# Kernel optimization log

Measured on AMD Instinct MI355X. Metric: run time of the kernel, lower is better.

## Reference

```python
import jax, jax.numpy as jnp
import numpy as np

D_MODEL = 1024
HEAD_SIZE = 64
BLOCK_SIZE = 2048
B, T = 4, 2048


def setup_inputs() -> dict:
    key = jax.random.key(0)
    ks = jax.random.split(key, 7)
    s = 1.0 / np.sqrt(D_MODEL)
    x = jax.random.normal(ks[0], (B, T, D_MODEL), dtype=jnp.float32)
    Wq = jax.random.uniform(ks[1], (D_MODEL, HEAD_SIZE), jnp.float32, -s, s)
    bq = jax.random.uniform(ks[2], (HEAD_SIZE,), jnp.float32, -s, s)
    Wk = jax.random.uniform(ks[3], (D_MODEL, HEAD_SIZE), jnp.float32, -s, s)
    bk = jax.random.uniform(ks[4], (HEAD_SIZE,), jnp.float32, -s, s)
    Wv = jax.random.uniform(ks[5], (D_MODEL, HEAD_SIZE), jnp.float32, -s, s)
    return {"x": x, "Wq": Wq, "bq": bq, "Wk": Wk, "bk": bk, "Wv": Wv, "mask": 1}


def reference(x, Wq, bq, Wk, bk, Wv, mask):
    # x: [B, T, C]; single attention head, dropout is identity (eval/p=0)
    Tlen = x.shape[1]
    q = x @ Wq + bq              # [B, T, hs]
    k = x @ Wk + bk              # [B, T, hs]
    v = x @ Wv                   # [B, T, hs] (no bias)
    hs = k.shape[-1]
    # Faithful to source: weights = QK^T / hs**(-0.5)  ==  QK^T * sqrt(hs)
    w = jnp.einsum('btd,bsd->bts', q, k) * jnp.sqrt(jnp.asarray(hs, x.dtype))
    if mask:
        causal = jnp.tril(jnp.ones((Tlen, Tlen), dtype=bool))
        w = jnp.where(causal, w, jnp.asarray(-jnp.inf, w.dtype))
    w = jax.nn.softmax(w, axis=-1)
    out = jnp.einsum('bts,bsd->btd', w, v)  # [B, T, hs]
    return out
```

## Files before the change

kernel.cpp:

```cpp
#include <hip/hip_runtime.h>
#include <hip/hip_bf16.h>

#define D_MODEL 1024
#define HS 64
#define T_LEN 2048
#define JCH 256
#define NCH 8

typedef __attribute__((ext_vector_type(8))) short bf16x8;
typedef __attribute__((ext_vector_type(4))) float f32x4;

__device__ inline void split8(const float* v, int4& hi, int4& lo) {
    union { unsigned short u[8]; int4 v4; } uh, ul;
    #pragma unroll
    for (int i = 0; i < 8; ++i) {
        const unsigned int b = __float_as_uint(v[i]);
        const unsigned short h = (unsigned short)(b >> 16);
        const float r = v[i] - __uint_as_float((unsigned int)h << 16);
        uh.u[i] = h;
        ul.u[i] = (unsigned short)(__float_as_uint(r) >> 16);
    }
    hi = uh.v4; lo = ul.v4;
}

__device__ inline unsigned short f2bf_rne(float f) {
    const unsigned int b = __float_as_uint(f);
    return (unsigned short)((b + 0x7FFFu + ((b >> 16) & 1u)) >> 16);
}
__device__ inline float bf2f(unsigned short h) {
    return __uint_as_float((unsigned int)h << 16);
}

__global__ __launch_bounds__(256) void wprep_kernel(
    const float* __restrict__ Wq, const float* __restrict__ Wk,
    const float* __restrict__ Wv, short* __restrict__ Wh, short* __restrict__ Wl)
{
    __shared__ float tile[64][69];
    const int tid = threadIdx.x;
    const int kb = blockIdx.x & 15;
    const int m  = blockIdx.x >> 4;
    const float* W = (m == 0) ? Wq : (m == 1) ? Wk : Wv;
    #pragma unroll
    for (int it = 0; it < 4; ++it) {
        const int idx = tid + 256 * it;
        const int kr = idx >> 4, c4 = idx & 15;
        *(float4*)&tile[kr][4 * c4] =
            *(const float4*)(W + (size_t)(kb * 64 + kr) * HS + 4 * c4);
    }
    __syncthreads();
    #pragma unroll
    for (int it = 0; it < 2; ++it) {
        const int s = tid + 256 * it;
        const int n = s >> 3, kc = s & 7;
        float v[8];
        #pragma unroll
        for (int i = 0; i < 8; ++i) v[i] = tile[kc * 8 + i][n];
        int4 hi, lo;
        split8(v, hi, lo);
        const size_t off = (size_t)(m * 64 + n) * D_MODEL + kb * 64 + kc * 8;
        *(int4*)(Wh + off) = hi;
        *(int4*)(Wl + off) = lo;
    }
}

__global__ __launch_bounds__(256, 3) void qkv_kernel(
    const float* __restrict__ x,
    const short* __restrict__ Wh, const short* __restrict__ Wl,
    const float* __restrict__ bq, const float* __restrict__ bk,
    float* __restrict__ q, float* __restrict__ k, float* __restrict__ vt, int BT)
{
    __shared__ __align__(16) short Ah[4 * 520], Al[4 * 520];
    __shared__ __align__(16) short Bh[8 * 520], Bl[8 * 520];

    const int tid  = threadIdx.x;
    const int r0   = blockIdx.x * 32;
    const int nb   = blockIdx.y;
    const int wave = tid >> 6;
    const int lane = tid & 63;
    const int mt_w = wave >> 1;
    const int nt0  = (wave & 1) * 2;

    f32x4 acc0 = (f32x4)(0.f);
    f32x4 acc1 = (f32x4)(0.f);

    const int amt = tid >> 7, akc = (tid >> 6) & 1, aln = tid & 63;
    const float* axsrc =
        x + (size_t)(r0 + amt * 16 + (aln & 15)) * D_MODEL + akc * 32 + (aln >> 4) * 8;

    const int b0nt = tid >> 7, b0kc = (tid >> 6) & 1, b0ln = tid & 63;
    const size_t b0off =
        (size_t)(nb * 64 + b0nt * 16 + (b0ln & 15)) * D_MODEL + b0kc * 32 + (b0ln >> 4) * 8;
    const int b1nt = 2 + (tid >> 7);
    const size_t b1off =
        (size_t)(nb * 64 + b1nt * 16 + (b0ln & 15)) * D_MODEL + b0kc * 32 + (b0ln >> 4) * 8;

    float4 a0v = *(const float4*)(axsrc);
    float4 a1v = *(const float4*)(axsrc + 4);
    int4 pb0h = *(const int4*)(Wh + b0off);
    int4 pb0l = *(const int4*)(Wl + b0off);
    int4 pb1h = *(const int4*)(Wh + b1off);
    int4 pb1l = *(const int4*)(Wl + b1off);

    for (int k0 = 0; k0 < D_MODEL; k0 += 64) {
        __syncthreads();
        {
            float xv[8];
            *(float4*)&xv[0] = a0v;
            *(float4*)&xv[4] = a1v;
            int4 hi, lo;
            split8(xv, hi, lo);
            *(int4*)&Ah[(amt * 2 + akc) * 520 + aln * 8] = hi;
            *(int4*)&Al[(amt * 2 + akc) * 520 + aln * 8] = lo;
        }
        *(int4*)&Bh[(b0nt * 2 + b0kc) * 520 + b0ln * 8] = pb0h;
        *(int4*)&Bl[(b0nt * 2 + b0kc) * 520 + b0ln * 8] = pb0l;
        *(int4*)&Bh[(b1nt * 2 + b0kc) * 520 + b0ln * 8] = pb1h;
        *(int4*)&Bl[(b1nt * 2 + b0kc) * 520 + b0ln * 8] = pb1l;
        __syncthreads();
        const int kn = k0 + 64;
        if (kn < D_MODEL) {
            a0v = *(const float4*)(axsrc + kn);
            a1v = *(const float4*)(axsrc + kn + 4);
            pb0h = *(const int4*)(Wh + b0off + kn);
            pb0l = *(const int4*)(Wl + b0off + kn);
            pb1h = *(const int4*)(Wh + b1off + kn);
            pb1l = *(const int4*)(Wl + b1off + kn);
        }
        #pragma unroll
        for (int kc = 0; kc < 2; ++kc) {
            const bf16x8 afh = *(const bf16x8*)&Ah[(mt_w * 2 + kc) * 520 + lane * 8];
            const bf16x8 afl = *(const bf16x8*)&Al[(mt_w * 2 + kc) * 520 + lane * 8];
            {
                const bf16x8 bfh = *(const bf16x8*)&Bh[(nt0 * 2 + kc) * 520 + lane * 8];
                const bf16x8 bfl = *(const bf16x8*)&Bl[(nt0 * 2 + kc) * 520 + lane * 8];
                acc0 = __builtin_amdgcn_mfma_f32_16x16x32_bf16(afh, bfh, acc0, 0, 0, 0);
                acc0 = __builtin_amdgcn_mfma_f32_16x16x32_bf16(afh, bfl, acc0, 0, 0, 0);
                acc0 = __builtin_amdgcn_mfma_f32_16x16x32_bf16(afl, bfh, acc0, 0, 0, 0);
            }
            {
                const bf16x8 bfh = *(const bf16x8*)&Bh[((nt0 + 1) * 2 + kc) * 520 + lane * 8];
                const bf16x8 bfl = *(const bf16x8*)&Bl[((nt0 + 1) * 2 + kc) * 520 + lane * 8];
                acc1 = __builtin_amdgcn_mfma_f32_16x16x32_bf16(afh, bfh, acc1, 0, 0, 0);
                acc1 = __builtin_amdgcn_mfma_f32_16x16x32_bf16(afh, bfl, acc1, 0, 0, 0);
                acc1 = __builtin_amdgcn_mfma_f32_16x16x32_bf16(afl, bfh, acc1, 0, 0, 0);
            }
        }
    }

    const int rowb = r0 + mt_w * 16 + (lane >> 4) * 4;
    #pragma unroll
    for (int j = 0; j < 2; ++j) {
        const f32x4 a = (j == 0) ? acc0 : acc1;
        const int c = nb * 64 + (nt0 + j) * 16 + (lane & 15);
        if (c < 64) {
            const float bias = bq[c];
            #pragma unroll
            for (int r = 0; r < 4; ++r)
                q[(size_t)(rowb + r) * HS + c] = a[r] + bias;
        } else if (c < 128) {
            const float bias = bk[c - 64];
            #pragma unroll
            for (int r = 0; r < 4; ++r)
                k[(size_t)(rowb + r) * HS + (c - 64)] = a[r] + bias;
        } else {
            float4 o;
            o.x = a[0]; o.y = a[1]; o.z = a[2]; o.w = a[3];
            *(float4*)(vt + (size_t)(c - 128) * BT + rowb) = o;
        }
    }
}

__global__ __launch_bounds__(256) void attn_kernel(
    const float* __restrict__ q_ws, const float* __restrict__ k_ws,
    const float* __restrict__ vt_ws, const int* __restrict__ maskp,
    float* __restrict__ part_O, float* __restrict__ part_ml, int BT)
{
    __shared__ __align__(16) short Kh[4096], Kl[4096];
    __shared__ __align__(16) short Vt[4096];
    __shared__ __align__(16) short Pl[4][16 * 72];

    const int tile  = blockIdx.x;
    const int chunk = blockIdx.y;
    const int r0 = tile * 64;
    const int tb = r0 / T_LEN;
    const int t0 = r0 - tb * T_LEN;
    const int mask = (*maskp != 0);
    const int n_max = mask ? (t0 + 64) : T_LEN;
    const int j0 = chunk * JCH;
    if (j0 >= n_max) return;
    const int hi_j = min(j0 + JCH, n_max);
    const int njt = (hi_j - j0 + 63) >> 6;

    const int tid  = threadIdx.x;
    const int w    = tid >> 6;
    const int lane = tid & 63;
    const int quad = lane >> 4;
    const int l15  = lane & 15;
    const int rw0  = t0 + 16 * w;
    const int rowa = r0 + 16 * w + quad * 4;

    bf16x8 qfh[2], qfl[2];
    {
        const float* qrow = q_ws + (size_t)(r0 + 16 * w + l15) * HS + quad * 8;
        #pragma unroll
        for (int kc = 0; kc < 2; ++kc) {
            float v[8];
            *(float4*)&v[0] = *(const float4*)(qrow + kc * 32);
            *(float4*)&v[4] = *(const float4*)(qrow + kc * 32 + 4);
            union { int4 i; bf16x8 b; } ch, cl;
            split8(v, ch.i, cl.i);
            qfh[kc] = ch.b;
            qfl[kc] = cl.b;
        }
    }

    f32x4 oacc[4];
    #pragma unroll
    for (int nt = 0; nt < 4; ++nt) oacc[nt] = (f32x4)(0.f);
    float m_r[4] = {-INFINITY, -INFINITY, -INFINITY, -INFINITY};
    float l_r[4] = {0.f, 0.f, 0.f, 0.f};

    const float* kbase = k_ws + (size_t)tb * T_LEN * HS;

    for (int jt = 0; jt < njt; ++jt) {
        const int jbase = j0 + jt * 64;
        __syncthreads();
        #pragma unroll
        for (int it = 0; it < 2; ++it) {
            const int s  = tid + 256 * it;
            const int ls = s & 63;
            const int sc = s >> 6;
            const int jsub = sc >> 1, kc = sc & 1;
            const int jrow = jbase + jsub * 16 + (ls & 15);
            const int koff = kc * 32 + (ls >> 4) * 8;
            const float* src = kbase + (size_t)jrow * HS + koff;
            float v[8];
            *(float4*)&v[0] = *(const float4*)src;
            *(float4*)&v[4] = *(const float4*)(src + 4);
            int4 hi, lo;
            split8(v, hi, lo);
            *(int4*)&Kh[s * 8] = hi;
            *(int4*)&Kl[s * 8] = lo;
        }
        #pragma unroll
        for (int it = 0; it < 2; ++it) {
            const int s  = tid + 256 * it;
            const int ls = s & 63;
            const int sc = s >> 6;
            const int jc = sc >> 2, nt = sc & 3;
            const int n  = nt * 16 + (ls & 15);
            const int jcol = jbase + jc * 32 + (ls >> 4) * 8;
            const float* src = vt_ws + (size_t)n * BT + tb * T_LEN + jcol;
            float v[8];
            *(float4*)&v[0] = *(const float4*)src;
            *(float4*)&v[4] = *(const float4*)(src + 4);
            union { unsigned short u[8]; int4 i; } pk;
            #pragma unroll
            for (int i = 0; i < 8; ++i) pk.u[i] = f2bf_rne(v[i]);
            *(int4*)&Vt[s * 8] = pk.i;
        }
        __syncthreads();

        const bool active = (!mask) || (jbase <= rw0 + 15);
        if (active) {
            f32x4 sacc[4];
            #pragma unroll
            for (int jsub = 0; jsub < 4; ++jsub) {
                f32x4 s = (f32x4)(0.f);
                #pragma unroll
                for (int kc = 0; kc < 2; ++kc) {
                    const bf16x8 kh = *(const bf16x8*)&Kh[((jsub * 2 + kc) * 64 + lane) * 8];
                    const bf16x8 kl = *(const bf16x8*)&Kl[((jsub * 2 + kc) * 64 + lane) * 8];
                    s = __builtin_amdgcn_mfma_f32_16x16x32_bf16(qfh[kc], kh, s, 0, 0, 0);
                    s = __builtin_amdgcn_mfma_f32_16x16x32_bf16(qfh[kc], kl, s, 0, 0, 0);
                    s = __builtin_amdgcn_mfma_f32_16x16x32_bf16(qfl[kc], kh, s, 0, 0, 0);
                }
                sacc[jsub] = s;
            }
            float sval[4][4], rmax[4];
            #pragma unroll
            for (int r = 0; r < 4; ++r) rmax[r] = -INFINITY;
            #pragma unroll
            for (int jsub = 0; jsub < 4; ++jsub) {
                const int jg = jbase + jsub * 16 + l15;
                #pragma unroll
                for (int r = 0; r < 4; ++r) {
                    const int tg = rw0 + quad * 4 + r;
                    const float vv = (mask && (jg > tg)) ? -INFINITY : 8.0f * sacc[jsub][r];
                    sval[jsub][r] = vv;
                    rmax[r] = fmaxf(rmax[r], vv);
                }
            }
            #pragma unroll
            for (int d = 1; d < 16; d <<= 1)
                #pragma unroll
                for (int r = 0; r < 4; ++r)
                    rmax[r] = fmaxf(rmax[r], __shfl_xor(rmax[r], d));
            float alpha[4], msafe[4];
            #pragma unroll
            for (int r = 0; r < 4; ++r) {
                const float mn = fmaxf(m_r[r], rmax[r]);
                msafe[r] = (mn == -INFINITY) ? 0.f : mn;
                alpha[r] = __expf(m_r[r] - msafe[r]);
                m_r[r] = mn;
            }
            short* Pw = &Pl[w][0];
            float rsum[4] = {0.f, 0.f, 0.f, 0.f};
            #pragma unroll
            for (int jsub = 0; jsub < 4; ++jsub) {
                #pragma unroll
                for (int r = 0; r < 4; ++r) {
                    const float e = __expf(sval[jsub][r] - msafe[r]);
                    const unsigned short eb = f2bf_rne(e);
                    Pw[(quad * 4 + r) * 72 + jsub * 16 + l15] = (short)eb;
                    rsum[r] += bf2f(eb);
                }
            }
            #pragma unroll
            for (int d = 1; d < 16; d <<= 1)
                #pragma unroll
                for (int r = 0; r < 4; ++r)
                    rsum[r] += __shfl_xor(rsum[r], d);
            #pragma unroll
            for (int r = 0; r < 4; ++r)
                l_r[r] = l_r[r] * alpha[r] + rsum[r];
            #pragma unroll
            for (int nt = 0; nt < 4; ++nt)
                #pragma unroll
                for (int r = 0; r < 4; ++r)
                    oacc[nt][r] *= alpha[r];
            bf16x8 pf[2];
            #pragma unroll
            for (int jc = 0; jc < 2; ++jc)
                pf[jc] = *(const bf16x8*)&Pw[l15 * 72 + jc * 32 + quad * 8];
            #pragma unroll
            for (int nt = 0; nt < 4; ++nt) {
                #pragma unroll
                for (int jc = 0; jc < 2; ++jc) {
                    const bf16x8 vf = *(const bf16x8*)&Vt[((jc * 4 + nt) * 64 + lane) * 8];
                    oacc[nt] = __builtin_amdgcn_mfma_f32_16x16x32_bf16(pf[jc], vf, oacc[nt], 0, 0, 0);
                }
            }
        }
    }

    #pragma unroll
    for (int nt = 0; nt < 4; ++nt)
        #pragma unroll
        for (int r = 0; r < 4; ++r)
            part_O[((size_t)(rowa + r) * NCH + chunk) * HS + nt * 16 + l15] = oacc[nt][r];
    if (l15 == 0) {
        #pragma unroll
        for (int r = 0; r < 4; ++r) {
            float2 ml;
            ml.x = m_r[r];
            ml.y = l_r[r];
            *(float2*)(part_ml + ((size_t)(rowa + r) * NCH + chunk) * 2) = ml;
        }
    }
}

__global__ __launch_bounds__(256) void combine_kernel(
    const float* __restrict__ part_O, const float* __restrict__ part_ml,
    const int* __restrict__ maskp, float* __restrict__ out)
{
    const int f = blockIdx.x * 256 + threadIdx.x;
    const int row = f >> 6;
    const int d = f & 63;
    const int t = row & (T_LEN - 1);
    const int mask = (*maskp != 0);
    const int n = mask ? (t + 1) : T_LEN;
    const int nc = (n + JCH - 1) / JCH;

    const float2* mlp = (const float2*)(part_ml + (size_t)row * NCH * 2);
    float M = -INFINITY;
    for (int c = 0; c < nc; ++c) M = fmaxf(M, mlp[c].x);
    float L = 0.f, O = 0.f;
    for (int c = 0; c < nc; ++c) {
        const float2 ml = mlp[c];
        const float w = __expf(ml.x - M);
        L += ml.y * w;
        O = fmaf(part_O[((size_t)row * NCH + c) * HS + d], w, O);
    }
    out[(size_t)row * HS + d] = O / L;
}

extern "C" void kernel_launch(void* const* d_in, const int* in_sizes, int n_in,
                              void* d_out, int out_size, void* d_ws, size_t ws_size,
                              hipStream_t stream) {
    const float* x  = (const float*)d_in[0];
    const float* Wq = (const float*)d_in[1];
    const float* bq = (const float*)d_in[2];
    const float* Wk = (const float*)d_in[3];
    const float* bk = (const float*)d_in[4];
    const float* Wv = (const float*)d_in[5];
    const int* maskp = (const int*)d_in[6];

    const int BT = in_sizes[0] / D_MODEL;

    float* q   = (float*)d_ws;
    float* k   = q + (size_t)BT * HS;
    float* vt  = k + (size_t)BT * HS;
    float* pO  = vt + (size_t)BT * HS;
    float* pml = pO + (size_t)BT * NCH * HS;

    short* Wh = (short*)pO;
    short* Wl = Wh + (size_t)192 * D_MODEL;

    wprep_kernel<<<48, 256, 0, stream>>>(Wq, Wk, Wv, Wh, Wl);
    dim3 qgrid(BT / 32, 3);
    qkv_kernel<<<qgrid, 256, 0, stream>>>(x, Wh, Wl, bq, bk, q, k, vt, BT);
    dim3 agrid(BT / 64, NCH);
    attn_kernel<<<agrid, 256, 0, stream>>>(q, k, vt, maskp, pO, pml, BT);
    combine_kernel<<<(BT * HS) / 256, 256, 0, stream>>>(pO, pml, maskp, (float*)d_out);
}
```

Before: 155.2 us.

## Pre-split x into fragment-layout bf16 hi/lo and async-copy tiles to LDS

The prep kernel now converts x, as well as the weights, into bf16 hi/lo pairs stored in MFMA fragment order. The QKV GEMM then streams those pre-split tiles straight into LDS with global_load_lds instead of splitting fp32 x in registers three times (once per N block). The attention split-K chunk count is also halved (JCH 512, NCH 4), which cuts partial-result traffic and combine work. The cost is an extra full pass writing 2x bf16 copies of x to workspace, attention parallelism reduced by half, and no register prefetch overlap in the GEMM loop.

```diff
diff --git a/kernel.cpp b/kernel.cpp
--- a/kernel.cpp
+++ b/kernel.cpp
@@ -4,8 +4,8 @@
 #define D_MODEL 1024
 #define HS 64
 #define T_LEN 2048
-#define JCH 256
-#define NCH 8
+#define JCH 512
+#define NCH 4
 
 typedef __attribute__((ext_vector_type(8))) short bf16x8;
 typedef __attribute__((ext_vector_type(4))) float f32x4;
@@ -31,46 +31,84 @@
     return __uint_as_float((unsigned int)h << 16);
 }
 
-__global__ __launch_bounds__(256) void wprep_kernel(
+__device__ inline void async_copy16(const short* g, short* l) {
+    __builtin_amdgcn_global_load_lds(
+        (const __attribute__((address_space(1))) void*)g,
+        (__attribute__((address_space(3))) void*)l, 16, 0, 0);
+}
+
+__global__ __launch_bounds__(256) void prep_kernel(
+    const float* __restrict__ x,
     const float* __restrict__ Wq, const float* __restrict__ Wk,
-    const float* __restrict__ Wv, short* __restrict__ Wh, short* __restrict__ Wl)
+    const float* __restrict__ Wv,
+    short* __restrict__ xh, short* __restrict__ xl,
+    short* __restrict__ wh, short* __restrict__ wl, int BT)
 {
     __shared__ float tile[64][69];
     const int tid = threadIdx.x;
-    const int kb = blockIdx.x & 15;
-    const int m  = blockIdx.x >> 4;
-    const float* W = (m == 0) ? Wq : (m == 1) ? Wk : Wv;
-    #pragma unroll
-    for (int it = 0; it < 4; ++it) {
-        const int idx = tid + 256 * it;
-        const int kr = idx >> 4, c4 = idx & 15;
-        *(float4*)&tile[kr][4 * c4] =
-            *(const float4*)(W + (size_t)(kb * 64 + kr) * HS + 4 * c4);
-    }
-    __syncthreads();
-    #pragma unroll
-    for (int it = 0; it < 2; ++it) {
-        const int s = tid + 256 * it;
-        const int n = s >> 3, kc = s & 7;
-        float v[8];
-        #pragma unroll
-        for (int i = 0; i < 8; ++i) v[i] = tile[kc * 8 + i][n];
-        int4 hi, lo;
-        split8(v, hi, lo);
-        const size_t off = (size_t)(m * 64 + n) * D_MODEL + kb * 64 + kc * 8;
-        *(int4*)(Wh + off) = hi;
-        *(int4*)(Wl + off) = lo;
-    }
-}
-
-__global__ __launch_bounds__(256, 3) void qkv_kernel(
-    const float* __restrict__ x,
-    const short* __restrict__ Wh, const short* __restrict__ Wl,
+    const int bx  = blockIdx.x;
+    const int nxb = BT >> 4;
+
+    if (bx < nxb) {
+        const int mtg = bx;
+        #pragma unroll
+        for (int i = 0; i < 8; ++i) {
+            const int s    = tid + 256 * i;
+            const int kc   = s >> 6;
+            const int lane = s & 63;
+            const float* src = x + (size_t)(mtg * 16 + (lane & 15)) * D_MODEL
+                                 + kc * 32 + (lane >> 4) * 8;
+            float v[8];
+            *(float4*)&v[0] = *(const float4*)src;
+            *(float4*)&v[4] = *(const float4*)(src + 4);
+            int4 hi, lo;
+            split8(v, hi, lo);
+            const size_t off = ((size_t)(mtg * 32 + kc) * 64 + lane) * 8;
+            *(int4*)(xh + off) = hi;
+            *(int4*)(xl + off) = lo;
+        }
+    } else {
+        const int wb = bx - nxb;
+        const int kb = wb & 15;
+        const int m  = wb >> 4;
+        const float* W = (m == 0) ? Wq : (m == 1) ? Wk : Wv;
+        #pragma unroll
+        for (int it = 0; it < 4; ++it) {
+            const int idx = tid + 256 * it;
+            const int kr = idx >> 4, c4 = idx & 15;
+            *(float4*)&tile[kr][4 * c4] =
+                *(const float4*)(W + (size_t)(kb * 64 + kr) * HS + 4 * c4);
+        }
+        __syncthreads();
+        #pragma unroll
+        for (int i = 0; i < 2; ++i) {
+            const int s    = tid + 256 * i;
+            const int ntl  = s >> 7;
+            const int kcl  = (s >> 6) & 1;
+            const int lane = s & 63;
+            const int n    = ntl * 16 + (lane & 15);
+            const int krel = kcl * 32 + (lane >> 4) * 8;
+            float v[8];
+            #pragma unroll
+            for (int e = 0; e < 8; ++e) v[e] = tile[krel + e][n];
+            int4 hi, lo;
+            split8(v, hi, lo);
+            const size_t off =
+                ((size_t)((m * 4 + ntl) * 32 + kb * 2 + kcl) * 64 + lane) * 8;
+            *(int4*)(wh + off) = hi;
+            *(int4*)(wl + off) = lo;
+        }
+    }
+}
+
+__global__ __launch_bounds__(256) void qkv_kernel(
+    const short* __restrict__ xh, const short* __restrict__ xl,
+    const short* __restrict__ wh, const short* __restrict__ wl,
     const float* __restrict__ bq, const float* __restrict__ bk,
     float* __restrict__ q, float* __restrict__ k, float* __restrict__ vt, int BT)
 {
-    __shared__ __align__(16) short Ah[4 * 520], Al[4 * 520];
-    __shared__ __align__(16) short Bh[8 * 520], Bl[8 * 520];
+    __shared__ __align__(16) short A_lds[8 * 512];
+    __shared__ __align__(16) short B_lds[16 * 512];
 
     const int tid  = threadIdx.x;
     const int r0   = blockIdx.x * 32;
@@ -83,63 +121,43 @@
     f32x4 acc0 = (f32x4)(0.f);
     f32x4 acc1 = (f32x4)(0.f);
 
-    const int amt = tid >> 7, akc = (tid >> 6) & 1, aln = tid & 63;
-    const float* axsrc =
-        x + (size_t)(r0 + amt * 16 + (aln & 15)) * D_MODEL + akc * 32 + (aln >> 4) * 8;
-
-    const int b0nt = tid >> 7, b0kc = (tid >> 6) & 1, b0ln = tid & 63;
-    const size_t b0off =
-        (size_t)(nb * 64 + b0nt * 16 + (b0ln & 15)) * D_MODEL + b0kc * 32 + (b0ln >> 4) * 8;
-    const int b1nt = 2 + (tid >> 7);
-    const size_t b1off =
-        (size_t)(nb * 64 + b1nt * 16 + (b0ln & 15)) * D_MODEL + b0kc * 32 + (b0ln >> 4) * 8;
-
-    float4 a0v = *(const float4*)(axsrc);
-    float4 a1v = *(const float4*)(axsrc + 4);
-    int4 pb0h = *(const int4*)(Wh + b0off);
-    int4 pb0l = *(const int4*)(Wl + b0off);
-    int4 pb1h = *(const int4*)(Wh + b1off);
-    int4 pb1l = *(const int4*)(Wl + b1off);
+    const size_t mtg0 = (size_t)(r0 >> 4);
+    const size_t ntg0 = (size_t)(nb * 4);
 
     for (int k0 = 0; k0 < D_MODEL; k0 += 64) {
+        const int kc0 = k0 >> 5;
         __syncthreads();
-        {
-            float xv[8];
-            *(float4*)&xv[0] = a0v;
-            *(float4*)&xv[4] = a1v;
-            int4 hi, lo;
-            split8(xv, hi, lo);
-            *(int4*)&Ah[(amt * 2 + akc) * 520 + aln * 8] = hi;
-            *(int4*)&Al[(amt * 2 + akc) * 520 + aln * 8] = lo;
-        }
-        *(int4*)&Bh[(b0nt * 2 + b0kc) * 520 + b0ln * 8] = pb0h;
-        *(int4*)&Bl[(b0nt * 2 + b0kc) * 520 + b0ln * 8] = pb0l;
-        *(int4*)&Bh[(b1nt * 2 + b0kc) * 520 + b0ln * 8] = pb1h;
-        *(int4*)&Bl[(b1nt * 2 + b0kc) * 520 + b0ln * 8] = pb1l;
+        #pragma unroll
+        for (int ii = 0; ii < 6; ++ii) {
+            const int g = wave * 6 + ii;
+            if (g < 8) {
+                const int mt = g >> 2, kcl = (g >> 1) & 1, p = g & 1;
+                const short* base = p ? xl : xh;
+                const short* gsrc = base + ((mtg0 + mt) * 32 + kc0 + kcl) * 512;
+                async_copy16(gsrc + lane * 8, &A_lds[g * 512]);
+            } else {
+                const int gb = g - 8;
+                const int nt = gb >> 2, kcl = (gb >> 1) & 1, p = gb & 1;
+                const short* base = p ? wl : wh;
+                const short* gsrc = base + ((ntg0 + nt) * 32 + kc0 + kcl) * 512;
+                async_copy16(gsrc + lane * 8, &B_lds[gb * 512]);
+            }
+        }
         __syncthreads();
-        const int kn = k0 + 64;
-        if (kn < D_MODEL) {
-            a0v = *(const float4*)(axsrc + kn);
-            a1v = *(const float4*)(axsrc + kn + 4);
-            pb0h = *(const int4*)(Wh + b0off + kn);
-            pb0l = *(const int4*)(Wl + b0off + kn);
-            pb1h = *(const int4*)(Wh + b1off + kn);
-            pb1l = *(const int4*)(Wl + b1off + kn);
-        }
-        #pragma unroll
-        for (int kc = 0; kc < 2; ++kc) {
-            const bf16x8 afh = *(const bf16x8*)&Ah[(mt_w * 2 + kc) * 520 + lane * 8];
-            const bf16x8 afl = *(const bf16x8*)&Al[(mt_w * 2 + kc) * 520 + lane * 8];
+        #pragma unroll
+        for (int kcl = 0; kcl < 2; ++kcl) {
+            const bf16x8 afh = *(const bf16x8*)&A_lds[(mt_w * 4 + kcl * 2 + 0) * 512 + lane * 8];
+            const bf16x8 afl = *(const bf16x8*)&A_lds[(mt_w * 4 + kcl * 2 + 1) * 512 + lane * 8];
             {
-                const bf16x8 bfh = *(const bf16x8*)&Bh[(nt0 * 2 + kc) * 520 + lane * 8];
-                const bf16x8 bfl = *(const bf16x8*)&Bl[(nt0 * 2 + kc) * 520 + lane * 8];
+                const bf16x8 bfh = *(const bf16x8*)&B_lds[(nt0 * 4 + kcl * 2 + 0) * 512 + lane * 8];
+                const bf16x8 bfl = *(const bf16x8*)&B_lds[(nt0 * 4 + kcl * 2 + 1) * 512 + lane * 8];
                 acc0 = __builtin_amdgcn_mfma_f32_16x16x32_bf16(afh, bfh, acc0, 0, 0, 0);
                 acc0 = __builtin_amdgcn_mfma_f32_16x16x32_bf16(afh, bfl, acc0, 0, 0, 0);
                 acc0 = __builtin_amdgcn_mfma_f32_16x16x32_bf16(afl, bfh, acc0, 0, 0, 0);
             }
             {
-                const bf16x8 bfh = *(const bf16x8*)&Bh[((nt0 + 1) * 2 + kc) * 520 + lane * 8];
-                const bf16x8 bfl = *(const bf16x8*)&Bl[((nt0 + 1) * 2 + kc) * 520 + lane * 8];
+                const bf16x8 bfh = *(const bf16x8*)&B_lds[((nt0 + 1) * 4 + kcl * 2 + 0) * 512 + lane * 8];
+                const bf16x8 bfl = *(const bf16x8*)&B_lds[((nt0 + 1) * 4 + kcl * 2 + 1) * 512 + lane * 8];
                 acc1 = __builtin_amdgcn_mfma_f32_16x16x32_bf16(afh, bfh, acc1, 0, 0, 0);
                 acc1 = __builtin_amdgcn_mfma_f32_16x16x32_bf16(afh, bfl, acc1, 0, 0, 0);
                 acc1 = __builtin_amdgcn_mfma_f32_16x16x32_bf16(afl, bfh, acc1, 0, 0, 0);
@@ -403,13 +421,14 @@
     float* vt  = k + (size_t)BT * HS;
     float* pO  = vt + (size_t)BT * HS;
     float* pml = pO + (size_t)BT * NCH * HS;
-
-    short* Wh = (short*)pO;
-    short* Wl = Wh + (size_t)192 * D_MODEL;
-
-    wprep_kernel<<<48, 256, 0, stream>>>(Wq, Wk, Wv, Wh, Wl);
+    short* xh  = (short*)(pml + (size_t)BT * NCH * 2);
+    short* xl  = xh + (size_t)BT * D_MODEL;
+    short* wh  = xl + (size_t)BT * D_MODEL;
+    short* wl  = wh + (size_t)192 * D_MODEL;
+
+    prep_kernel<<<BT / 16 + 48, 256, 0, stream>>>(x, Wq, Wk, Wv, xh, xl, wh, wl, BT);
     dim3 qgrid(BT / 32, 3);
-    qkv_kernel<<<qgrid, 256, 0, stream>>>(x, Wh, Wl, bq, bk, q, k, vt, BT);
+    qkv_kernel<<<qgrid, 256, 0, stream>>>(xh, xl, wh, wl, bq, bk, q, k, vt, BT);
     dim3 agrid(BT / 64, NCH);
     attn_kernel<<<agrid, 256, 0, stream>>>(q, k, vt, maskp, pO, pml, BT);
     combine_kernel<<<(BT * HS) / 256, 256, 0, stream>>>(pO, pml, maskp, (float*)d_out);
```

Result: faster. 143.8 us (-7.3%).
